# Performance work log

Measured on AMD Instinct MI355X. Metric: run time of the kernel, lower is better.

## Reference

```python
import jax, jax.numpy as jnp
import numpy as np

BS, C_IN, L = 64, 64, 4096
C_OUT, KS, K, RATIO = 128, 7, 4, 4
HIDDEN = C_IN // RATIO
PAD, TEMP = 3, 30.0


def setup_inputs() -> dict:
    key = jax.random.key(0)
    k1, k2, k3, k4, k5 = jax.random.split(key, 5)
    x = jax.random.normal(k1, (BS, C_IN, L), dtype=jnp.float32)
    # attention 1x1 convs stored as matmul matrices
    w_attn1 = jax.random.normal(k2, (HIDDEN, C_IN), dtype=jnp.float32) * (2.0 / C_IN) ** 0.5
    w_attn2 = jax.random.normal(k3, (K, HIDDEN), dtype=jnp.float32) * (2.0 / HIDDEN) ** 0.5
    # K-bank conv weights [K, out, in, ks] and biases [K, out]
    weight = jax.random.normal(k4, (K, C_OUT, C_IN, KS), dtype=jnp.float32) * 0.05
    bias = jax.random.normal(k5, (K, C_OUT), dtype=jnp.float32) * 0.05
    return {"x": x, "w_attn1": w_attn1, "w_attn2": w_attn2, "weight": weight, "bias": bias}


def reference(x, w_attn1, w_attn2, weight, bias):
    # Attention1d: global avg pool -> 1x1 conv -> relu -> 1x1 conv -> softmax(./T)
    pooled = jnp.mean(x, axis=-1)                      # [bs, C_in]
    h = jax.nn.relu(pooled @ w_attn1.T)                # [bs, hidden]
    logits = h @ w_attn2.T                             # [bs, K]
    att = jax.nn.softmax(logits / TEMP, axis=-1)       # [bs, K]

    # softmax-weighted aggregation of the K weight banks -> per-sample kernels
    agg_w = jnp.einsum('bk,koif->boif', att, weight)   # [bs, out, in, ks]
    agg_b = att @ bias                                 # [bs, out]

    # per-sample conv1d (the grouped-conv trick), vectorized with vmap
    def conv_one(xi, wi):
        # xi: [C_in, L], wi: [out, in, ks]
        return jax.lax.conv_general_dilated(
            xi[None], wi, window_strides=(1,), padding=[(PAD, PAD)],
            dimension_numbers=('NCH', 'OIH', 'NCH'))[0]  # [out, L]

    out = jax.vmap(conv_one)(x, agg_w) + agg_b[:, :, None]  # [bs, out, L]
    return out
```

## Files before the change

### kernel.cpp

```cpp
#include <hip/hip_runtime.h>

typedef __bf16 bf16;
typedef __bf16 bf16x8 __attribute__((ext_vector_type(8)));
typedef __bf16 bf16x2 __attribute__((ext_vector_type(2)));
typedef float f32x4 __attribute__((ext_vector_type(4)));

#define BS 64
#define CI 64
#define LEN 4096
#define CO 128
#define KS 7
#define NK 4
#define HID 16
#define TEMP 30.0f

#define KTOT 448
#define WROW 456
#define WBAT (CO * WROW)
#define XROW 72
#define XC 134
#define LTILE 128
#define TPB 8

__global__ void pool_kernel(const float* __restrict__ x, float* __restrict__ pooled) {
    int bc = blockIdx.x;
    const float4* xp = (const float4*)(x + (size_t)bc * LEN);
    int t = threadIdx.x;
    float s = 0.f;
#pragma unroll
    for (int j = 0; j < 4; ++j) {
        float4 v = xp[t + 256 * j];
        s += (v.x + v.y) + (v.z + v.w);
    }
#pragma unroll
    for (int off = 32; off > 0; off >>= 1) s += __shfl_down(s, off, 64);
    __shared__ float red[4];
    if ((t & 63) == 0) red[t >> 6] = s;
    __syncthreads();
    if (t == 0) pooled[bc] = (red[0] + red[1] + red[2] + red[3]) * (1.0f / LEN);
}

__global__ void attn_kernel(const float* __restrict__ pooled,
                            const float* __restrict__ w1,
                            const float* __restrict__ w2,
                            const float* __restrict__ bias,
                            float* __restrict__ att_g,
                            float* __restrict__ aggb_g) {
    int b = blockIdx.x, t = threadIdx.x;
    __shared__ float p[CI], h[HID], att[NK];
    if (t < CI) p[t] = pooled[b * CI + t];
    __syncthreads();
    if (t < HID) {
        float s = 0.f;
        for (int i = 0; i < CI; ++i) s += p[i] * w1[t * CI + i];
        h[t] = fmaxf(s, 0.f);
    }
    __syncthreads();
    if (t == 0) {
        float lg[NK];
        float m = -1e30f;
        for (int k = 0; k < NK; ++k) {
            float s = 0.f;
            for (int j = 0; j < HID; ++j) s += h[j] * w2[k * HID + j];
            lg[k] = s * (1.0f / TEMP);
            m = fmaxf(m, lg[k]);
        }
        float e[NK], tot = 0.f;
        for (int k = 0; k < NK; ++k) { e[k] = expf(lg[k] - m); tot += e[k]; }
        float inv = 1.0f / tot;
        for (int k = 0; k < NK; ++k) { att[k] = e[k] * inv; att_g[b * NK + k] = att[k]; }
    }
    __syncthreads();
    if (t < CO) {
        float s = 0.f;
        for (int k = 0; k < NK; ++k) s += att[k] * bias[k * CO + t];
        aggb_g[b * CO + t] = s;
    }
}

__global__ void aggw_kernel(const float* __restrict__ weight,
                            const float* __restrict__ att_g,
                            bf16* __restrict__ wagg) {
    int o = blockIdx.x >> 1;
    int bh = blockIdx.x & 1;
    int t = threadIdx.x;
    __shared__ float lw[4 * KTOT];
    __shared__ __align__(16) float attl[128];

    const float* wo = weight + o * KTOT;
    for (int idx = t; idx < 4 * KTOT; idx += 256) {
        int bank = idx / KTOT;
        int r = idx - bank * KTOT;
        lw[idx] = wo[(size_t)bank * (CO * KTOT) + r];
    }
    if (t < 128) attl[t] = att_g[bh * 128 + t];
    __syncthreads();

    if (t < 224) {
        float w8[8];
#pragma unroll
        for (int j = 0; j < 2; ++j) {
            int kout = 2 * t + j;
            int i = kout & 63, f = kout >> 6;
#pragma unroll
            for (int bank = 0; bank < 4; ++bank)
                w8[j * 4 + bank] = lw[bank * KTOT + i * KS + f];
        }
        for (int bb = 0; bb < 32; ++bb) {
            int b = bh * 32 + bb;
            float4 a = *(const float4*)&attl[bb * 4];
            float v0 = a.x * w8[0] + a.y * w8[1] + a.z * w8[2] + a.w * w8[3];
            float v1 = a.x * w8[4] + a.y * w8[5] + a.z * w8[6] + a.w * w8[7];
            bf16x2 pk; pk[0] = (bf16)v0; pk[1] = (bf16)v1;
            *(bf16x2*)(wagg + (size_t)b * WBAT + o * WROW + 2 * t) = pk;
        }
    }
}

struct XStage { float4 m[8]; float e1, e2; };

__global__ __launch_bounds__(256, 2) void conv_kernel(
    const float* __restrict__ x,
    const bf16* __restrict__ wagg,
    const float* __restrict__ aggb,
    float* __restrict__ out) {
    __shared__ __align__(16) bf16 lds_x[2][XC * XROW];

    int nwg = gridDim.x;
    int bid = blockIdx.x;
    int logical = (bid & 7) * (nwg >> 3) + (bid >> 3);
    int b = logical >> 3;
    int rem = logical & 7;
    int oh = rem >> 2, lsp = rem & 3;

    int t = threadIdx.x;
    int lane = t & 63, wid = t >> 6;
    int ln = lane & 15, g = lane >> 4;
    int wm = wid >> 1, wn = wid & 1;

    const bf16* wgb = wagg + (size_t)b * WBAT
                    + (size_t)(oh * 64 + wm * 32 + ln) * WROW + g * 8;
    bf16x8 av[2][14];
#pragma unroll
    for (int mf = 0; mf < 2; ++mf)
#pragma unroll
        for (int kk = 0; kk < 14; ++kk)
            av[mf][kk] = *(const bf16x8*)(wgb + mf * 16 * WROW + kk * 32);

    int l0base = lsp * (LTILE * TPB);
    int si = t >> 2, sf = t & 3;
    const float* xb = x + (size_t)b * CI * LEN;

    auto load_x = [&](int l0, XStage& s) {
#pragma unroll
        for (int j = 0; j < 8; ++j) {
            int c4 = sf + 4 * j;
            s.m[j] = *(const float4*)(xb + (size_t)si * LEN + l0 + 4 * c4);
        }
        int i1 = t / 6, s1 = t - i1 * 6;
        int c1 = (s1 < 3) ? s1 : (128 + s1);
        int gl1 = l0 - 3 + c1;
        s.e1 = (gl1 >= 0 && gl1 < LEN) ? xb[(size_t)i1 * LEN + gl1] : 0.f;
        s.e2 = 0.f;
        if (t < 128) {
            int e2 = 256 + t, i2 = e2 / 6, s2 = e2 - i2 * 6;
            int c2 = (s2 < 3) ? s2 : (128 + s2);
            int gl2 = l0 - 3 + c2;
            s.e2 = (gl2 >= 0 && gl2 < LEN) ? xb[(size_t)i2 * LEN + gl2] : 0.f;
        }
    };
    auto write_x = [&](int buf, const XStage& s) {
        bf16* lb = lds_x[buf];
#pragma unroll
        for (int j = 0; j < 8; ++j) {
            int c4 = sf + 4 * j;
#pragma unroll
            for (int dl = 0; dl < 4; ++dl) {
                float v = (&s.m[j].x)[dl];
                lb[(4 * c4 + 3 + dl) * XROW + si] = (bf16)v;
            }
        }
        int i1 = t / 6, s1 = t - i1 * 6;
        int c1 = (s1 < 3) ? s1 : (128 + s1);
        lb[c1 * XROW + i1] = (bf16)s.e1;
        if (t < 128) {
            int e2 = 256 + t, i2 = e2 / 6, s2 = e2 - i2 * 6;
            int c2 = (s2 < 3) ? s2 : (128 + s2);
            lb[c2 * XROW + i2] = (bf16)s.e2;
        }
    };

    float bias_r[2][4];
    int orow_off[2][4];
#pragma unroll
    for (int mf = 0; mf < 2; ++mf)
#pragma unroll
        for (int r = 0; r < 4; ++r) {
            int o = oh * 64 + wm * 32 + mf * 16 + g * 4 + r;
            bias_r[mf][r] = aggb[b * CO + o];
            orow_off[mf][r] = (b * CO + o) * LEN;
        }

    XStage s0;
    load_x(l0base, s0);
    write_x(0, s0);
    __syncthreads();

    for (int tl = 0; tl < TPB; ++tl) {
        int l0 = l0base + tl * LTILE;
        XStage sn;
        if (tl + 1 < TPB) load_x(l0 + LTILE, sn);

        f32x4 acc[2][4];
#pragma unroll
        for (int mf = 0; mf < 2; ++mf)
#pragma unroll
            for (int nf = 0; nf < 4; ++nf)
                acc[mf][nf] = (f32x4){0.f, 0.f, 0.f, 0.f};

        const bf16* bp = lds_x[tl & 1] + (wn * 64 + ln) * XROW + g * 8;

#pragma unroll
        for (int kk = 0; kk < 14; ++kk) {
            int boff = (kk >> 1) * XROW + (kk & 1) * 32;
            bf16x8 bv[4];
#pragma unroll
            for (int nf = 0; nf < 4; ++nf)
                bv[nf] = *(const bf16x8*)(bp + nf * 16 * XROW + boff);
#pragma unroll
            for (int mf = 0; mf < 2; ++mf)
#pragma unroll
                for (int nf = 0; nf < 4; ++nf)
                    acc[mf][nf] = __builtin_amdgcn_mfma_f32_16x16x32_bf16(
                        av[mf][kk], bv[nf], acc[mf][nf], 0, 0, 0);
        }

#pragma unroll
        for (int mf = 0; mf < 2; ++mf)
#pragma unroll
            for (int nf = 0; nf < 4; ++nf) {
                int l = l0 + wn * 64 + nf * 16 + ln;
#pragma unroll
                for (int r = 0; r < 4; ++r)
                    out[(size_t)orow_off[mf][r] + l] = acc[mf][nf][r] + bias_r[mf][r];
            }

        if (tl + 1 < TPB) {
            write_x((tl + 1) & 1, sn);
            __syncthreads();
        }
    }
}

extern "C" void kernel_launch(void* const* d_in, const int* in_sizes, int n_in,
                              void* d_out, int out_size, void* d_ws, size_t ws_size,
                              hipStream_t stream) {
    const float* x  = (const float*)d_in[0];
    const float* w1 = (const float*)d_in[1];
    const float* w2 = (const float*)d_in[2];
    const float* wt = (const float*)d_in[3];
    const float* bs = (const float*)d_in[4];
    float* out = (float*)d_out;

    bf16* wagg = (bf16*)d_ws;
    float* pooled = (float*)((char*)d_ws + (size_t)BS * WBAT * 2);
    float* att_g  = pooled + BS * CI;
    float* aggb   = att_g + BS * NK;

    pool_kernel<<<BS * CI, 256, 0, stream>>>(x, pooled);
    attn_kernel<<<BS, 256, 0, stream>>>(pooled, w1, w2, bs, att_g, aggb);
    aggw_kernel<<<CO * 2, 256, 0, stream>>>(wt, att_g, wagg);
    conv_kernel<<<BS * 8, 256, 0, stream>>>(x, wagg, aggb, out);
}
```

Baseline: 64.99 us.

## Fuse attention into weight aggregation and restructure conv with 32x32 MFMA tiles

The attention MLP is folded into the weight-aggregation kernel, with each block recomputing attention for its 32 samples, and the bias aggregation moves into the conv kernel. This drops one launch. The conv kernel now gives each block all 128 output channels over 64-wide L tiles, using 32x32x16 bf16 MFMAs and loading the halo as whole float4 rows with guarded edge loads. The x tile is therefore reused across all output channels instead of being loaded twice. In exchange the attention MLP is computed redundantly across blocks, and each thread holds more weight registers, which may limit occupancy.

```diff
diff --git a/kernel.cpp b/kernel.cpp
--- a/kernel.cpp
+++ b/kernel.cpp
@@ -3,7 +3,7 @@
 typedef __bf16 bf16;
 typedef __bf16 bf16x8 __attribute__((ext_vector_type(8)));
 typedef __bf16 bf16x2 __attribute__((ext_vector_type(2)));
-typedef float f32x4 __attribute__((ext_vector_type(4)));
+typedef float f32x16 __attribute__((ext_vector_type(16)));
 
 #define BS 64
 #define CI 64
@@ -18,8 +18,8 @@
 #define WROW 456
 #define WBAT (CO * WROW)
 #define XROW 72
-#define XC 134
-#define LTILE 128
+#define XC 80
+#define LTILE 64
 #define TPB 8
 
 __global__ void pool_kernel(const float* __restrict__ x, float* __restrict__ pooled) {
@@ -40,60 +40,59 @@
     if (t == 0) pooled[bc] = (red[0] + red[1] + red[2] + red[3]) * (1.0f / LEN);
 }
 
-__global__ void attn_kernel(const float* __restrict__ pooled,
+__global__ void aggw_kernel(const float* __restrict__ pooled,
                             const float* __restrict__ w1,
                             const float* __restrict__ w2,
-                            const float* __restrict__ bias,
+                            const float* __restrict__ weight,
                             float* __restrict__ att_g,
-                            float* __restrict__ aggb_g) {
-    int b = blockIdx.x, t = threadIdx.x;
-    __shared__ float p[CI], h[HID], att[NK];
-    if (t < CI) p[t] = pooled[b * CI + t];
-    __syncthreads();
-    if (t < HID) {
-        float s = 0.f;
-        for (int i = 0; i < CI; ++i) s += p[i] * w1[t * CI + i];
-        h[t] = fmaxf(s, 0.f);
-    }
-    __syncthreads();
-    if (t == 0) {
-        float lg[NK];
-        float m = -1e30f;
-        for (int k = 0; k < NK; ++k) {
-            float s = 0.f;
-            for (int j = 0; j < HID; ++j) s += h[j] * w2[k * HID + j];
-            lg[k] = s * (1.0f / TEMP);
-            m = fmaxf(m, lg[k]);
-        }
-        float e[NK], tot = 0.f;
-        for (int k = 0; k < NK; ++k) { e[k] = expf(lg[k] - m); tot += e[k]; }
-        float inv = 1.0f / tot;
-        for (int k = 0; k < NK; ++k) { att[k] = e[k] * inv; att_g[b * NK + k] = att[k]; }
-    }
-    __syncthreads();
-    if (t < CO) {
-        float s = 0.f;
-        for (int k = 0; k < NK; ++k) s += att[k] * bias[k * CO + t];
-        aggb_g[b * CO + t] = s;
-    }
-}
-
-__global__ void aggw_kernel(const float* __restrict__ weight,
-                            const float* __restrict__ att_g,
                             bf16* __restrict__ wagg) {
     int o = blockIdx.x >> 1;
     int bh = blockIdx.x & 1;
     int t = threadIdx.x;
+    __shared__ float p[32 * 64];
+    __shared__ float hsh[32 * 16];
+    __shared__ float att_s[32][4];
     __shared__ float lw[4 * KTOT];
-    __shared__ __align__(16) float attl[128];
-
-    const float* wo = weight + o * KTOT;
+
+    const float* wo = weight + (size_t)o * KTOT;
     for (int idx = t; idx < 4 * KTOT; idx += 256) {
         int bank = idx / KTOT;
         int r = idx - bank * KTOT;
         lw[idx] = wo[(size_t)bank * (CO * KTOT) + r];
     }
-    if (t < 128) attl[t] = att_g[bh * 128 + t];
+    for (int idx = t; idx < 32 * 64; idx += 256) p[idx] = pooled[bh * 2048 + idx];
+    __syncthreads();
+
+    {
+        int bb = t >> 3, h2 = (t & 7) * 2;
+#pragma unroll
+        for (int u = 0; u < 2; ++u) {
+            int hh = h2 + u;
+            float s = 0.f;
+            for (int i = 0; i < 64; ++i) s += p[bb * 64 + i] * w1[hh * 64 + i];
+            hsh[bb * 16 + hh] = fmaxf(s, 0.f);
+        }
+    }
+    __syncthreads();
+    if (t < 32) {
+        float lg[NK], m = -1e30f;
+#pragma unroll
+        for (int k = 0; k < NK; ++k) {
+            float s = 0.f;
+            for (int j = 0; j < HID; ++j) s += hsh[t * 16 + j] * w2[k * HID + j];
+            lg[k] = s * (1.0f / TEMP);
+            m = fmaxf(m, lg[k]);
+        }
+        float e[NK], tot = 0.f;
+#pragma unroll
+        for (int k = 0; k < NK; ++k) { e[k] = expf(lg[k] - m); tot += e[k]; }
+        float inv = 1.0f / tot;
+#pragma unroll
+        for (int k = 0; k < NK; ++k) {
+            att_s[t][k] = e[k] * inv;
+            if (blockIdx.x < 2) att_g[(bh * 32 + t) * NK + k] = e[k] * inv;
+        }
+    }
     __syncthreads();
 
     if (t < 224) {
@@ -108,142 +107,122 @@
         }
         for (int bb = 0; bb < 32; ++bb) {
             int b = bh * 32 + bb;
-            float4 a = *(const float4*)&attl[bb * 4];
-            float v0 = a.x * w8[0] + a.y * w8[1] + a.z * w8[2] + a.w * w8[3];
-            float v1 = a.x * w8[4] + a.y * w8[5] + a.z * w8[6] + a.w * w8[7];
+            float a0 = att_s[bb][0], a1 = att_s[bb][1];
+            float a2 = att_s[bb][2], a3 = att_s[bb][3];
+            float v0 = a0 * w8[0] + a1 * w8[1] + a2 * w8[2] + a3 * w8[3];
+            float v1 = a0 * w8[4] + a1 * w8[5] + a2 * w8[6] + a3 * w8[7];
             bf16x2 pk; pk[0] = (bf16)v0; pk[1] = (bf16)v1;
             *(bf16x2*)(wagg + (size_t)b * WBAT + o * WROW + 2 * t) = pk;
         }
     }
 }
 
-struct XStage { float4 m[8]; float e1, e2; };
+struct XStage { float4 m[5]; };
 
 __global__ __launch_bounds__(256, 2) void conv_kernel(
     const float* __restrict__ x,
     const bf16* __restrict__ wagg,
-    const float* __restrict__ aggb,
+    const float* __restrict__ att_g,
+    const float* __restrict__ bias,
     float* __restrict__ out) {
     __shared__ __align__(16) bf16 lds_x[2][XC * XROW];
+    __shared__ float aggb_l[CO];
 
     int nwg = gridDim.x;
     int bid = blockIdx.x;
     int logical = (bid & 7) * (nwg >> 3) + (bid >> 3);
     int b = logical >> 3;
-    int rem = logical & 7;
-    int oh = rem >> 2, lsp = rem & 3;
+    int lsp = logical & 7;
 
     int t = threadIdx.x;
     int lane = t & 63, wid = t >> 6;
-    int ln = lane & 15, g = lane >> 4;
-    int wm = wid >> 1, wn = wid & 1;
+    int l31 = lane & 31, hi = lane >> 5;
+
+    if (t < CO) {
+        float a0 = att_g[b * NK + 0], a1 = att_g[b * NK + 1];
+        float a2 = att_g[b * NK + 2], a3 = att_g[b * NK + 3];
+        aggb_l[t] = a0 * bias[0 * CO + t] + a1 * bias[1 * CO + t] +
+                    a2 * bias[2 * CO + t] + a3 * bias[3 * CO + t];
+    }
 
     const bf16* wgb = wagg + (size_t)b * WBAT
-                    + (size_t)(oh * 64 + wm * 32 + ln) * WROW + g * 8;
-    bf16x8 av[2][14];
-#pragma unroll
-    for (int mf = 0; mf < 2; ++mf)
-#pragma unroll
-        for (int kk = 0; kk < 14; ++kk)
-            av[mf][kk] = *(const bf16x8*)(wgb + mf * 16 * WROW + kk * 32);
+                    + (size_t)(wid * 32 + l31) * WROW + hi * 8;
+    bf16x8 av[28];
+#pragma unroll
+    for (int kk = 0; kk < 28; ++kk)
+        av[kk] = *(const bf16x8*)(wgb + kk * 16);
 
     int l0base = lsp * (LTILE * TPB);
     int si = t >> 2, sf = t & 3;
     const float* xb = x + (size_t)b * CI * LEN;
 
-    auto load_x = [&](int l0, XStage& s) {
-#pragma unroll
-        for (int j = 0; j < 8; ++j) {
-            int c4 = sf + 4 * j;
-            s.m[j] = *(const float4*)(xb + (size_t)si * LEN + l0 + 4 * c4);
-        }
-        int i1 = t / 6, s1 = t - i1 * 6;
-        int c1 = (s1 < 3) ? s1 : (128 + s1);
-        int gl1 = l0 - 3 + c1;
-        s.e1 = (gl1 >= 0 && gl1 < LEN) ? xb[(size_t)i1 * LEN + gl1] : 0.f;
-        s.e2 = 0.f;
-        if (t < 128) {
-            int e2 = 256 + t, i2 = e2 / 6, s2 = e2 - i2 * 6;
-            int c2 = (s2 < 3) ? s2 : (128 + s2);
-            int gl2 = l0 - 3 + c2;
-            s.e2 = (gl2 >= 0 && gl2 < LEN) ? xb[(size_t)i2 * LEN + gl2] : 0.f;
+    auto load_x = [&](int l0, XStage& s, bool guard) {
+        int g0 = l0 - 8;
+        if (!guard) {
+#pragma unroll
+            for (int m = 0; m < 5; ++m)
+                s.m[m] = *(const float4*)(xb + (size_t)si * LEN + g0 + 20 * sf + 4 * m);
+        } else {
+#pragma unroll
+            for (int m = 0; m < 5; ++m) {
+                int cb = g0 + 20 * sf + 4 * m;
+#pragma unroll
+                for (int e = 0; e < 4; ++e) {
+                    int c = cb + e;
+                    (&s.m[m].x)[e] = (c >= 0 && c < LEN) ? xb[(size_t)si * LEN + c] : 0.f;
+                }
+            }
         }
     };
     auto write_x = [&](int buf, const XStage& s) {
         bf16* lb = lds_x[buf];
 #pragma unroll
-        for (int j = 0; j < 8; ++j) {
-            int c4 = sf + 4 * j;
-#pragma unroll
-            for (int dl = 0; dl < 4; ++dl) {
-                float v = (&s.m[j].x)[dl];
-                lb[(4 * c4 + 3 + dl) * XROW + si] = (bf16)v;
+        for (int m = 0; m < 5; ++m)
+#pragma unroll
+            for (int e = 0; e < 4; ++e) {
+                int c = 20 * sf + 4 * m + e;
+                lb[c * XROW + si] = (bf16)((&s.m[m].x)[e]);
             }
-        }
-        int i1 = t / 6, s1 = t - i1 * 6;
-        int c1 = (s1 < 3) ? s1 : (128 + s1);
-        lb[c1 * XROW + i1] = (bf16)s.e1;
-        if (t < 128) {
-            int e2 = 256 + t, i2 = e2 / 6, s2 = e2 - i2 * 6;
-            int c2 = (s2 < 3) ? s2 : (128 + s2);
-            lb[c2 * XROW + i2] = (bf16)s.e2;
-        }
     };
 
-    float bias_r[2][4];
-    int orow_off[2][4];
-#pragma unroll
-    for (int mf = 0; mf < 2; ++mf)
-#pragma unroll
-        for (int r = 0; r < 4; ++r) {
-            int o = oh * 64 + wm * 32 + mf * 16 + g * 4 + r;
-            bias_r[mf][r] = aggb[b * CO + o];
-            orow_off[mf][r] = (b * CO + o) * LEN;
-        }
-
     XStage s0;
-    load_x(l0base, s0);
+    load_x(l0base, s0, lsp == 0);
     write_x(0, s0);
     __syncthreads();
+
+    float bias_r[16];
+#pragma unroll
+    for (int reg = 0; reg < 16; ++reg)
+        bias_r[reg] = aggb_l[wid * 32 + (reg & 3) + 8 * (reg >> 2) + 4 * hi];
+
+    size_t orow0 = ((size_t)(b * CO + wid * 32)) * LEN;
 
     for (int tl = 0; tl < TPB; ++tl) {
         int l0 = l0base + tl * LTILE;
         XStage sn;
-        if (tl + 1 < TPB) load_x(l0 + LTILE, sn);
-
-        f32x4 acc[2][4];
-#pragma unroll
-        for (int mf = 0; mf < 2; ++mf)
-#pragma unroll
-            for (int nf = 0; nf < 4; ++nf)
-                acc[mf][nf] = (f32x4){0.f, 0.f, 0.f, 0.f};
-
-        const bf16* bp = lds_x[tl & 1] + (wn * 64 + ln) * XROW + g * 8;
-
-#pragma unroll
-        for (int kk = 0; kk < 14; ++kk) {
-            int boff = (kk >> 1) * XROW + (kk & 1) * 32;
-            bf16x8 bv[4];
-#pragma unroll
-            for (int nf = 0; nf < 4; ++nf)
-                bv[nf] = *(const bf16x8*)(bp + nf * 16 * XROW + boff);
-#pragma unroll
-            for (int mf = 0; mf < 2; ++mf)
-#pragma unroll
-                for (int nf = 0; nf < 4; ++nf)
-                    acc[mf][nf] = __builtin_amdgcn_mfma_f32_16x16x32_bf16(
-                        av[mf][kk], bv[nf], acc[mf][nf], 0, 0, 0);
-        }
-
-#pragma unroll
-        for (int mf = 0; mf < 2; ++mf)
-#pragma unroll
-            for (int nf = 0; nf < 4; ++nf) {
-                int l = l0 + wn * 64 + nf * 16 + ln;
-#pragma unroll
-                for (int r = 0; r < 4; ++r)
-                    out[(size_t)orow_off[mf][r] + l] = acc[mf][nf][r] + bias_r[mf][r];
-            }
+        if (tl + 1 < TPB)
+            load_x(l0 + LTILE, sn, (lsp == 7) && (tl + 1 == TPB - 1));
+
+        f32x16 acc0 = {}, acc1 = {};
+        const bf16* lb = lds_x[tl & 1];
+        const bf16* bp = lb + (size_t)(l31 + 5) * XROW + hi * 8;
+
+#pragma unroll
+        for (int kk = 0; kk < 28; ++kk) {
+            int boff = (kk >> 2) * XROW + (kk & 3) * 16;
+            bf16x8 bv0 = *(const bf16x8*)(bp + boff);
+            bf16x8 bv1 = *(const bf16x8*)(bp + 32 * XROW + boff);
+            acc0 = __builtin_amdgcn_mfma_f32_32x32x16_bf16(av[kk], bv0, acc0, 0, 0, 0);
+            acc1 = __builtin_amdgcn_mfma_f32_32x32x16_bf16(av[kk], bv1, acc1, 0, 0, 0);
+        }
+
+#pragma unroll
+        for (int reg = 0; reg < 16; ++reg) {
+            int row = (reg & 3) + 8 * (reg >> 2) + 4 * hi;
+            size_t rbase = orow0 + (size_t)row * LEN + l0 + l31;
+            out[rbase] = acc0[reg] + bias_r[reg];
+            out[rbase + 32] = acc1[reg] + bias_r[reg];
+        }
 
         if (tl + 1 < TPB) {
             write_x((tl + 1) & 1, sn);
@@ -265,10 +244,8 @@
     bf16* wagg = (bf16*)d_ws;
     float* pooled = (float*)((char*)d_ws + (size_t)BS * WBAT * 2);
     float* att_g  = pooled + BS * CI;
-    float* aggb   = att_g + BS * NK;
 
     pool_kernel<<<BS * CI, 256, 0, stream>>>(x, pooled);
-    attn_kernel<<<BS, 256, 0, stream>>>(pooled, w1, w2, bs, att_g, aggb);
-    aggw_kernel<<<CO * 2, 256, 0, stream>>>(wt, att_g, wagg);
-    conv_kernel<<<BS * 8, 256, 0, stream>>>(x, wagg, aggb, out);
-}
+    aggw_kernel<<<CO * 2, 256, 0, stream>>>(pooled, w1, w2, wt, att_g, wagg);
+    conv_kernel<<<BS * 8, 256, 0, stream>>>(x, wagg, att_g, bs, out);
+}
```

Result: slower. 69.51 us (+7.0%).

## Fuse attention into weight aggregation, compute bias in conv, reorder LDS write before stores

Applied to the files above, without the earlier changes.

Removes the separate attention kernel launch by recomputing the pooled->MLP->softmax attention redundantly in every aggregation block. The aggregated bias is now computed inside the conv kernel from att and bias. The next x tile's LDS write and barrier are moved ahead of the output stores, so global stores can overlap the following tile. This trades a launch and a dependency for redundant small MLP compute per block.

```diff
diff --git a/kernel.cpp b/kernel.cpp
--- a/kernel.cpp
+++ b/kernel.cpp
@@ -40,60 +40,59 @@
     if (t == 0) pooled[bc] = (red[0] + red[1] + red[2] + red[3]) * (1.0f / LEN);
 }
 
-__global__ void attn_kernel(const float* __restrict__ pooled,
+__global__ void aggw_kernel(const float* __restrict__ pooled,
                             const float* __restrict__ w1,
                             const float* __restrict__ w2,
-                            const float* __restrict__ bias,
+                            const float* __restrict__ weight,
                             float* __restrict__ att_g,
-                            float* __restrict__ aggb_g) {
-    int b = blockIdx.x, t = threadIdx.x;
-    __shared__ float p[CI], h[HID], att[NK];
-    if (t < CI) p[t] = pooled[b * CI + t];
-    __syncthreads();
-    if (t < HID) {
-        float s = 0.f;
-        for (int i = 0; i < CI; ++i) s += p[i] * w1[t * CI + i];
-        h[t] = fmaxf(s, 0.f);
-    }
-    __syncthreads();
-    if (t == 0) {
-        float lg[NK];
-        float m = -1e30f;
-        for (int k = 0; k < NK; ++k) {
-            float s = 0.f;
-            for (int j = 0; j < HID; ++j) s += h[j] * w2[k * HID + j];
-            lg[k] = s * (1.0f / TEMP);
-            m = fmaxf(m, lg[k]);
-        }
-        float e[NK], tot = 0.f;
-        for (int k = 0; k < NK; ++k) { e[k] = expf(lg[k] - m); tot += e[k]; }
-        float inv = 1.0f / tot;
-        for (int k = 0; k < NK; ++k) { att[k] = e[k] * inv; att_g[b * NK + k] = att[k]; }
-    }
-    __syncthreads();
-    if (t < CO) {
-        float s = 0.f;
-        for (int k = 0; k < NK; ++k) s += att[k] * bias[k * CO + t];
-        aggb_g[b * CO + t] = s;
-    }
-}
-
-__global__ void aggw_kernel(const float* __restrict__ weight,
-                            const float* __restrict__ att_g,
                             bf16* __restrict__ wagg) {
     int o = blockIdx.x >> 1;
     int bh = blockIdx.x & 1;
     int t = threadIdx.x;
+    __shared__ float p[32 * 64];
+    __shared__ float hsh[32 * 16];
+    __shared__ float att_s[32][4];
     __shared__ float lw[4 * KTOT];
-    __shared__ __align__(16) float attl[128];
-
-    const float* wo = weight + o * KTOT;
+
+    const float* wo = weight + (size_t)o * KTOT;
     for (int idx = t; idx < 4 * KTOT; idx += 256) {
         int bank = idx / KTOT;
         int r = idx - bank * KTOT;
         lw[idx] = wo[(size_t)bank * (CO * KTOT) + r];
     }
-    if (t < 128) attl[t] = att_g[bh * 128 + t];
+    for (int idx = t; idx < 32 * 64; idx += 256) p[idx] = pooled[bh * 2048 + idx];
+    __syncthreads();
+
+    {
+        int bb = t >> 3, h2 = (t & 7) * 2;
+#pragma unroll
+        for (int u = 0; u < 2; ++u) {
+            int hh = h2 + u;
+            float s = 0.f;
+            for (int i = 0; i < 64; ++i) s += p[bb * 64 + i] * w1[hh * 64 + i];
+            hsh[bb * 16 + hh] = fmaxf(s, 0.f);
+        }
+    }
+    __syncthreads();
+    if (t < 32) {
+        float lg[NK], m = -1e30f;
+#pragma unroll
+        for (int k = 0; k < NK; ++k) {
+            float s = 0.f;
+            for (int j = 0; j < HID; ++j) s += hsh[t * 16 + j] * w2[k * HID + j];
+            lg[k] = s * (1.0f / TEMP);
+            m = fmaxf(m, lg[k]);
+        }
+        float e[NK], tot = 0.f;
+#pragma unroll
+        for (int k = 0; k < NK; ++k) { e[k] = expf(lg[k] - m); tot += e[k]; }
+        float inv = 1.0f / tot;
+#pragma unroll
+        for (int k = 0; k < NK; ++k) {
+            att_s[t][k] = e[k] * inv;
+            if (blockIdx.x < 2) att_g[(bh * 32 + t) * NK + k] = e[k] * inv;
+        }
+    }
     __syncthreads();
 
     if (t < 224) {
@@ -108,9 +107,10 @@
         }
         for (int bb = 0; bb < 32; ++bb) {
             int b = bh * 32 + bb;
-            float4 a = *(const float4*)&attl[bb * 4];
-            float v0 = a.x * w8[0] + a.y * w8[1] + a.z * w8[2] + a.w * w8[3];
-            float v1 = a.x * w8[4] + a.y * w8[5] + a.z * w8[6] + a.w * w8[7];
+            float a0 = att_s[bb][0], a1 = att_s[bb][1];
+            float a2 = att_s[bb][2], a3 = att_s[bb][3];
+            float v0 = a0 * w8[0] + a1 * w8[1] + a2 * w8[2] + a3 * w8[3];
+            float v1 = a0 * w8[4] + a1 * w8[5] + a2 * w8[6] + a3 * w8[7];
             bf16x2 pk; pk[0] = (bf16)v0; pk[1] = (bf16)v1;
             *(bf16x2*)(wagg + (size_t)b * WBAT + o * WROW + 2 * t) = pk;
         }
@@ -122,9 +122,11 @@
 __global__ __launch_bounds__(256, 2) void conv_kernel(
     const float* __restrict__ x,
     const bf16* __restrict__ wagg,
-    const float* __restrict__ aggb,
+    const float* __restrict__ att_g,
+    const float* __restrict__ bias,
     float* __restrict__ out) {
     __shared__ __align__(16) bf16 lds_x[2][XC * XROW];
+    __shared__ float aggb_l[CO];
 
     int nwg = gridDim.x;
     int bid = blockIdx.x;
@@ -137,6 +139,13 @@
     int lane = t & 63, wid = t >> 6;
     int ln = lane & 15, g = lane >> 4;
     int wm = wid >> 1, wn = wid & 1;
+
+    if (t < CO) {
+        float a0 = att_g[b * NK + 0], a1 = att_g[b * NK + 1];
+        float a2 = att_g[b * NK + 2], a3 = att_g[b * NK + 3];
+        aggb_l[t] = a0 * bias[0 * CO + t] + a1 * bias[1 * CO + t] +
+                    a2 * bias[2 * CO + t] + a3 * bias[3 * CO + t];
+    }
 
     const bf16* wgb = wagg + (size_t)b * WBAT
                     + (size_t)(oh * 64 + wm * 32 + ln) * WROW + g * 8;
@@ -190,21 +199,21 @@
         }
     };
 
-    float bias_r[2][4];
-    int orow_off[2][4];
-#pragma unroll
-    for (int mf = 0; mf < 2; ++mf)
-#pragma unroll
-        for (int r = 0; r < 4; ++r) {
-            int o = oh * 64 + wm * 32 + mf * 16 + g * 4 + r;
-            bias_r[mf][r] = aggb[b * CO + o];
-            orow_off[mf][r] = (b * CO + o) * LEN;
-        }
-
     XStage s0;
     load_x(l0base, s0);
     write_x(0, s0);
     __syncthreads();
+
+    float bias_r[2][4];
+    int orow_off[2][4];
+#pragma unroll
+    for (int mf = 0; mf < 2; ++mf)
+#pragma unroll
+        for (int r = 0; r < 4; ++r) {
+            int o = oh * 64 + wm * 32 + mf * 16 + g * 4 + r;
+            bias_r[mf][r] = aggb_l[o];
+            orow_off[mf][r] = (b * CO + o) * LEN;
+        }
 
     for (int tl = 0; tl < TPB; ++tl) {
         int l0 = l0base + tl * LTILE;
@@ -235,6 +244,11 @@
                         av[mf][kk], bv[nf], acc[mf][nf], 0, 0, 0);
         }
 
+        if (tl + 1 < TPB) {
+            write_x((tl + 1) & 1, sn);
+            __syncthreads();
+        }
+
 #pragma unroll
         for (int mf = 0; mf < 2; ++mf)
 #pragma unroll
@@ -244,11 +258,6 @@
                 for (int r = 0; r < 4; ++r)
                     out[(size_t)orow_off[mf][r] + l] = acc[mf][nf][r] + bias_r[mf][r];
             }
-
-        if (tl + 1 < TPB) {
-            write_x((tl + 1) & 1, sn);
-            __syncthreads();
-        }
     }
 }
 
@@ -265,10 +274,8 @@
     bf16* wagg = (bf16*)d_ws;
     float* pooled = (float*)((char*)d_ws + (size_t)BS * WBAT * 2);
     float* att_g  = pooled + BS * CI;
-    float* aggb   = att_g + BS * NK;
 
     pool_kernel<<<BS * CI, 256, 0, stream>>>(x, pooled);
-    attn_kernel<<<BS, 256, 0, stream>>>(pooled, w1, w2, bs, att_g, aggb);
-    aggw_kernel<<<CO * 2, 256, 0, stream>>>(wt, att_g, wagg);
-    conv_kernel<<<BS * 8, 256, 0, stream>>>(x, wagg, aggb, out);
-}
+    aggw_kernel<<<CO * 2, 256, 0, stream>>>(pooled, w1, w2, wt, att_g, wagg);
+    conv_kernel<<<BS * 8, 256, 0, stream>>>(x, wagg, att_g, bs, out);
+}
```

New measurement: 66.59 us. 2.5% more time.
